# Performance work log

Hardware: AMD Instinct MI355X
Metric: run time of the kernel (lower is better)

Reference implementation:

```python
import jax, jax.numpy as jnp
import numpy as np

BLOCK = 128


def setup_inputs() -> dict:
    key = jax.random.key(0)
    k_x, k_w, k_s, k_b = jax.random.split(key, 4)
    B, S, IN, OUT = 2, 2048, 4096, 4096
    x = jax.random.normal(k_x, (B, S, IN), dtype=jnp.float32)
    # fp8-quantized weight values (simulate e4m3 rounding, keep fp32 storage)
    w = jax.random.normal(k_w, (OUT, IN), dtype=jnp.float32) * 0.02
    weight = w.astype(jnp.float8_e4m3fn).astype(jnp.float32)
    # per-128x128-block inverse scales
    weight_scale_inv = jax.random.uniform(
        k_s, (OUT // BLOCK, IN // BLOCK), dtype=jnp.float32, minval=0.5, maxval=1.5)
    bias = jax.random.normal(k_b, (OUT,), dtype=jnp.float32) * 0.01
    return {"x": x, "weight": weight, "weight_scale_inv": weight_scale_inv, "bias": bias}


def _dequant(weight, scale_inv):
    # weight: [O, I], scale_inv: [O/128, I/128] -> broadcast each scale over a 128x128 block
    O, I = weight.shape
    w = weight.reshape(O // BLOCK, BLOCK, I // BLOCK, BLOCK)
    w = w * scale_inv[:, None, :, None]
    return w.reshape(O, I)


def reference(x, weight, weight_scale_inv, bias):
    w_deq = _dequant(weight, weight_scale_inv)          # [O, I]
    out = jnp.einsum('bsi,oi->bso', x, w_deq)           # [B, S, O]
    return out + bias
```

## Files before the change

### kernel.cpp

```cpp
#include <hip/hip_runtime.h>
#include <hip/hip_bf16.h>
#include <stdint.h>

typedef __attribute__((ext_vector_type(4))) float f32x4;
typedef __attribute__((ext_vector_type(8))) short short8;

__device__ __forceinline__ ushort f2b(float f) {
    union { __hip_bfloat16 h; ushort u; } c;
    c.h = __float2bfloat16(f);
    return c.u;
}

__device__ __forceinline__ void gload_lds16(const void* g, void* lds) {
    __builtin_amdgcn_global_load_lds((const __attribute__((address_space(1))) void*)g,
                                     (__attribute__((address_space(3))) void*)lds,
                                     16, 0, 0);
}

#define BARRIER()  asm volatile("s_barrier" ::: "memory")
#define LGKM0()    asm volatile("s_waitcnt lgkmcnt(0)" ::: "memory")
#define VMCNT2()   asm volatile("s_waitcnt vmcnt(2)" ::: "memory")

__global__ void conv_x_kernel(const float* __restrict__ x, ushort* __restrict__ xb, long n8) {
    long i = (long)blockIdx.x * blockDim.x + threadIdx.x;
    if (i >= n8) return;
    const float4* xv = (const float4*)x;
    float4 v0 = xv[i * 2], v1 = xv[i * 2 + 1];
    short8 r;
    r[0] = (short)f2b(v0.x); r[1] = (short)f2b(v0.y); r[2] = (short)f2b(v0.z); r[3] = (short)f2b(v0.w);
    r[4] = (short)f2b(v1.x); r[5] = (short)f2b(v1.y); r[6] = (short)f2b(v1.z); r[7] = (short)f2b(v1.w);
    *(short8*)&xb[i * 8] = r;
}

__global__ void conv_w_kernel(const float* __restrict__ w, const float* __restrict__ sinv,
                              ushort* __restrict__ wb, int K, int nbk) {
    const int o = blockIdx.y;
    const int c = (blockIdx.x * blockDim.x + threadIdx.x) * 8;
    if (c >= K) return;
    const float s = sinv[(o >> 7) * nbk + (c >> 7)];
    const float4* wv = (const float4*)(w + (size_t)o * K + c);
    float4 v0 = wv[0], v1 = wv[1];
    short8 r;
    r[0] = (short)f2b(v0.x * s); r[1] = (short)f2b(v0.y * s); r[2] = (short)f2b(v0.z * s); r[3] = (short)f2b(v0.w * s);
    r[4] = (short)f2b(v1.x * s); r[5] = (short)f2b(v1.y * s); r[6] = (short)f2b(v1.z * s); r[7] = (short)f2b(v1.w * s);
    *(short8*)&wb[(size_t)o * K + c] = r;
}

__global__ __launch_bounds__(512, 2)
void gemm256_kernel(const ushort* __restrict__ A, const ushort* __restrict__ Bm,
                    const float* __restrict__ bias, float* __restrict__ C,
                    int M, int N, int K) {
    __shared__ alignas(16) short sm[2][32768];

    const int tid  = threadIdx.x;
    const int lane = tid & 63;
    const int wid  = tid >> 6;
    const int wr   = wid >> 2;
    const int wc   = wid & 3;
    const int nbn  = N >> 8;

    const int nwg = gridDim.x;
    const int swz = (blockIdx.x & 7) * (nwg >> 3) + (blockIdx.x >> 3);
    const int bm  = swz / nbn;
    const int bn  = swz % nbn;

    const short* gA = (const short*)A + (size_t)bm * 256 * K;
    const short* gB = (const short*)Bm + (size_t)bn * 256 * K;

    const int srow = wid * 8 + (lane >> 3);
    const int scol = ((lane & 7) ^ (lane >> 3)) << 3;

    auto STAGE_A = [&](int U, int kt, int buf) {
        const short* src = gA + (size_t)(U * 64 + srow) * K + kt * 64 + scol;
        gload_lds16(src, &sm[buf][U * 4096 + wid * 512]);
    };
    auto STAGE_B = [&](int U, int kt, int buf) {
        const short* src = gB + (size_t)(U * 64 + srow) * K + kt * 64 + scol;
        gload_lds16(src, &sm[buf][16384 + U * 4096 + wid * 512]);
    };

    auto LD_A = [&](const short* Ab, int mh, int kk, short8 (&a)[4]) {
#pragma unroll
        for (int m = 0; m < 4; ++m) {
            int row = wr * 128 + mh * 64 + m * 16 + (lane & 15);
            a[m] = *(const short8*)&Ab[row * 64 + ((kk * 32 + (lane >> 4) * 8) ^ ((lane & 7) << 3))];
        }
    };
    auto LD_B = [&](const short* Bb, int kk, short8 (&b)[4]) {
#pragma unroll
        for (int n = 0; n < 4; ++n) {
            int row = wc * 64 + n * 16 + (lane & 15);
            b[n] = *(const short8*)&Bb[row * 64 + ((kk * 32 + (lane >> 4) * 8) ^ ((lane & 7) << 3))];
        }
    };

    f32x4 acc[8][4] = {};

    const int nkt = K >> 6;

    {
#pragma unroll
        for (int U = 0; U < 4; ++U) STAGE_A(U, 0, 0);
#pragma unroll
        for (int U = 0; U < 4; ++U) STAGE_B(U, 0, 0);
        const int t1 = (nkt > 1) ? 1 : 0;
        STAGE_A(0, t1, 1);
        STAGE_A(2, t1, 1);
        VMCNT2();
        BARRIER();
    }

    for (int t = 0; t < nkt; ++t) {
        const int b  = t & 1;
        const short* Ab = &sm[b][0];
        const short* Bb = &sm[b][16384];
        const int tn  = (t + 1 < nkt) ? t + 1 : nkt - 1;
        const int tnn = (t + 2 < nkt) ? t + 2 : nkt - 1;

        short8 a0[4], a1[4], bf0[4], bf1[4];

        LD_A(Ab, 0, 0, a0);
        LD_B(Bb, 0, bf0);
        STAGE_B(0, tn, b ^ 1); STAGE_B(1, tn, b ^ 1); STAGE_B(2, tn, b ^ 1); STAGE_B(3, tn, b ^ 1);
        BARRIER();
        __builtin_amdgcn_s_setprio(1);
#pragma unroll
        for (int m = 0; m < 4; ++m)
#pragma unroll
            for (int n = 0; n < 4; ++n)
                acc[m][n] = __builtin_amdgcn_mfma_f32_16x16x32_bf16(a0[m], bf0[n], acc[m][n], 0, 0, 0);
        __builtin_amdgcn_s_setprio(0);
        LGKM0();
        BARRIER();

        LD_A(Ab, 1, 0, a1);
        STAGE_A(1, tn, b ^ 1); STAGE_A(3, tn, b ^ 1);
        BARRIER();
        __builtin_amdgcn_s_setprio(1);
#pragma unroll
        for (int m = 0; m < 4; ++m)
#pragma unroll
            for (int n = 0; n < 4; ++n)
                acc[4 + m][n] = __builtin_amdgcn_mfma_f32_16x16x32_bf16(a1[m], bf0[n], acc[4 + m][n], 0, 0, 0);
        __builtin_amdgcn_s_setprio(0);
        LGKM0();
        BARRIER();

        LD_A(Ab, 0, 1, a0);
        LD_B(Bb, 1, bf1);
        BARRIER();
        __builtin_amdgcn_s_setprio(1);
#pragma unroll
        for (int m = 0; m < 4; ++m)
#pragma unroll
            for (int n = 0; n < 4; ++n)
                acc[m][n] = __builtin_amdgcn_mfma_f32_16x16x32_bf16(a0[m], bf1[n], acc[m][n], 0, 0, 0);
        __builtin_amdgcn_s_setprio(0);
        LGKM0();
        BARRIER();

        LD_A(Ab, 1, 1, a1);
        STAGE_A(0, tnn, b); STAGE_A(2, tnn, b);
        BARRIER();
        __builtin_amdgcn_s_setprio(1);
#pragma unroll
        for (int m = 0; m < 4; ++m)
#pragma unroll
            for (int n = 0; n < 4; ++n)
                acc[4 + m][n] = __builtin_amdgcn_mfma_f32_16x16x32_bf16(a1[m], bf1[n], acc[4 + m][n], 0, 0, 0);
        __builtin_amdgcn_s_setprio(0);
        LGKM0();
        VMCNT2();
        BARRIER();
    }

    const int r0 = bm * 256 + wr * 128 + (lane >> 4) * 4;
    const int c0 = bn * 256 + wc * 64 + (lane & 15);
#pragma unroll
    for (int n = 0; n < 4; ++n) {
        float bv = bias[c0 + n * 16];
#pragma unroll
        for (int m = 0; m < 8; ++m) {
#pragma unroll
            for (int r = 0; r < 4; ++r) {
                C[(size_t)(r0 + m * 16 + r) * N + (c0 + n * 16)] = acc[m][n][r] + bv;
            }
        }
    }
}

__global__ void fallback_gemm(const float* __restrict__ x, const float* __restrict__ w,
                              const float* __restrict__ sinv, const float* __restrict__ bias,
                              float* __restrict__ out, int M, int N, int K) {
    int n = blockIdx.x * 64 + (threadIdx.x & 63);
    int m = blockIdx.y * 4 + (threadIdx.x >> 6);
    if (m >= M || n >= N) return;
    const int nbk = K >> 7;
    float acc = 0.f;
    for (int k = 0; k < K; ++k)
        acc += x[(size_t)m * K + k] * w[(size_t)n * K + k] * sinv[(n >> 7) * nbk + (k >> 7)];
    out[(size_t)m * N + n] = acc + bias[n];
}

extern "C" void kernel_launch(void* const* d_in, const int* in_sizes, int n_in,
                              void* d_out, int out_size, void* d_ws, size_t ws_size,
                              hipStream_t stream) {
    const float* x    = (const float*)d_in[0];
    const float* w    = (const float*)d_in[1];
    const float* sinv = (const float*)d_in[2];
    const float* bias = (const float*)d_in[3];
    float* out        = (float*)d_out;

    const int O = in_sizes[3];
    const int K = in_sizes[1] / O;
    const int M = (int)((long)in_sizes[0] / K);
    const int N = O;

    const size_t need = ((size_t)M * K + (size_t)N * K) * sizeof(ushort);
    const int nwg = (M / 256) * (N / 256);
    const bool ok = ws_size >= need && (M % 256 == 0) && (N % 256 == 0) &&
                    (K % 128 == 0) && (nwg % 8 == 0) && ((long)M * K % 2048 == 0) &&
                    (K % 2048 == 0);
    if (ok) {
        ushort* xb = (ushort*)d_ws;
        ushort* wb = xb + (size_t)M * K;
        long n8 = (long)M * K / 8;
        conv_x_kernel<<<dim3((unsigned)(n8 / 256)), 256, 0, stream>>>(x, xb, n8);
        conv_w_kernel<<<dim3(K / 2048, N), 256, 0, stream>>>(w, sinv, wb, K, K >> 7);
        gemm256_kernel<<<dim3(nwg), 512, 0, stream>>>(xb, wb, bias, out, M, N, K);
    } else {
        dim3 g(N / 64, (M + 3) / 4);
        fallback_gemm<<<g, 256, 0, stream>>>(x, w, sinv, bias, out, M, N, K);
    }
}
```

Baseline: 293.0 us.

## Fuse fp32-to-bf16 conversion and dequant scaling into GEMM tile loading

Removes the separate x and weight conversion kernels and the bf16 workspace. The GEMM now loads fp32 tiles through registers, applies the block scale, converts to bf16 and writes swizzled LDS, with loads software-pipelined across the four MFMA phases. This saves the extra kernel launches and the bf16 round trip through global memory. In exchange, each tile reads twice the global bytes, conversion runs inside the main loop, register pressure rises, and the direct global-to-LDS loads are lost.

```diff
diff --git a/kernel.cpp b/kernel.cpp
--- a/kernel.cpp
+++ b/kernel.cpp
@@ -11,45 +11,15 @@
     return c.u;
 }
 
-__device__ __forceinline__ void gload_lds16(const void* g, void* lds) {
-    __builtin_amdgcn_global_load_lds((const __attribute__((address_space(1))) void*)g,
-                                     (__attribute__((address_space(3))) void*)lds,
-                                     16, 0, 0);
-}
-
 #define BARRIER()  asm volatile("s_barrier" ::: "memory")
 #define LGKM0()    asm volatile("s_waitcnt lgkmcnt(0)" ::: "memory")
-#define VMCNT2()   asm volatile("s_waitcnt vmcnt(2)" ::: "memory")
-
-__global__ void conv_x_kernel(const float* __restrict__ x, ushort* __restrict__ xb, long n8) {
-    long i = (long)blockIdx.x * blockDim.x + threadIdx.x;
-    if (i >= n8) return;
-    const float4* xv = (const float4*)x;
-    float4 v0 = xv[i * 2], v1 = xv[i * 2 + 1];
-    short8 r;
-    r[0] = (short)f2b(v0.x); r[1] = (short)f2b(v0.y); r[2] = (short)f2b(v0.z); r[3] = (short)f2b(v0.w);
-    r[4] = (short)f2b(v1.x); r[5] = (short)f2b(v1.y); r[6] = (short)f2b(v1.z); r[7] = (short)f2b(v1.w);
-    *(short8*)&xb[i * 8] = r;
-}
-
-__global__ void conv_w_kernel(const float* __restrict__ w, const float* __restrict__ sinv,
-                              ushort* __restrict__ wb, int K, int nbk) {
-    const int o = blockIdx.y;
-    const int c = (blockIdx.x * blockDim.x + threadIdx.x) * 8;
-    if (c >= K) return;
-    const float s = sinv[(o >> 7) * nbk + (c >> 7)];
-    const float4* wv = (const float4*)(w + (size_t)o * K + c);
-    float4 v0 = wv[0], v1 = wv[1];
-    short8 r;
-    r[0] = (short)f2b(v0.x * s); r[1] = (short)f2b(v0.y * s); r[2] = (short)f2b(v0.z * s); r[3] = (short)f2b(v0.w * s);
-    r[4] = (short)f2b(v1.x * s); r[5] = (short)f2b(v1.y * s); r[6] = (short)f2b(v1.z * s); r[7] = (short)f2b(v1.w * s);
-    *(short8*)&wb[(size_t)o * K + c] = r;
-}
+
+struct U8 { float4 lo, hi; };
 
 __global__ __launch_bounds__(512, 2)
-void gemm256_kernel(const ushort* __restrict__ A, const ushort* __restrict__ Bm,
-                    const float* __restrict__ bias, float* __restrict__ C,
-                    int M, int N, int K) {
+void gemm256_fused_kernel(const float* __restrict__ X, const float* __restrict__ W,
+                          const float* __restrict__ sinv, const float* __restrict__ bias,
+                          float* __restrict__ C, int M, int N, int K, int nbk) {
     __shared__ alignas(16) short sm[2][32768];
 
     const int tid  = threadIdx.x;
@@ -63,20 +33,39 @@
     const int swz = (blockIdx.x & 7) * (nwg >> 3) + (blockIdx.x >> 3);
     const int bm  = swz / nbn;
     const int bn  = swz % nbn;
-
-    const short* gA = (const short*)A + (size_t)bm * 256 * K;
-    const short* gB = (const short*)Bm + (size_t)bn * 256 * K;
+    const int bn2 = bn * 2;
+
+    const float* gA = X + (size_t)bm * 256 * K;
+    const float* gB = W + (size_t)bn * 256 * K;
 
     const int srow = wid * 8 + (lane >> 3);
-    const int scol = ((lane & 7) ^ (lane >> 3)) << 3;
-
-    auto STAGE_A = [&](int U, int kt, int buf) {
-        const short* src = gA + (size_t)(U * 64 + srow) * K + kt * 64 + scol;
-        gload_lds16(src, &sm[buf][U * 4096 + wid * 512]);
-    };
-    auto STAGE_B = [&](int U, int kt, int buf) {
-        const short* src = gB + (size_t)(U * 64 + srow) * K + kt * 64 + scol;
-        gload_lds16(src, &sm[buf][16384 + U * 4096 + wid * 512]);
+    const int scl8 = (lane & 7) * 8;
+    const int wOff = (wid * 8 + (lane >> 3)) * 64 + ((((lane & 7) ^ (lane >> 3))) << 3);
+
+    auto LOAD_A = [&](int U, int kt) -> U8 {
+        const float* p = gA + (size_t)(U * 64 + srow) * K + kt * 64 + scl8;
+        U8 r; r.lo = *(const float4*)p; r.hi = *(const float4*)(p + 4); return r;
+    };
+    auto LOAD_B = [&](int U, int kt) -> U8 {
+        const float* p = gB + (size_t)(U * 64 + srow) * K + kt * 64 + scl8;
+        U8 r; r.lo = *(const float4*)p; r.hi = *(const float4*)(p + 4); return r;
+    };
+    auto WRITE_A = [&](int U, int buf, const U8& v) {
+        short8 r;
+        r[0] = (short)f2b(v.lo.x); r[1] = (short)f2b(v.lo.y);
+        r[2] = (short)f2b(v.lo.z); r[3] = (short)f2b(v.lo.w);
+        r[4] = (short)f2b(v.hi.x); r[5] = (short)f2b(v.hi.y);
+        r[6] = (short)f2b(v.hi.z); r[7] = (short)f2b(v.hi.w);
+        *(short8*)&sm[buf][U * 4096 + wOff] = r;
+    };
+    auto WRITE_B = [&](int U, int kt, int buf, const U8& v) {
+        const float s = sinv[(bn2 + (U >> 1)) * nbk + (kt >> 1)];
+        short8 r;
+        r[0] = (short)f2b(v.lo.x * s); r[1] = (short)f2b(v.lo.y * s);
+        r[2] = (short)f2b(v.lo.z * s); r[3] = (short)f2b(v.lo.w * s);
+        r[4] = (short)f2b(v.hi.x * s); r[5] = (short)f2b(v.hi.y * s);
+        r[6] = (short)f2b(v.hi.z * s); r[7] = (short)f2b(v.hi.w * s);
+        *(short8*)&sm[buf][16384 + U * 4096 + wOff] = r;
     };
 
     auto LD_A = [&](const short* Ab, int mh, int kk, short8 (&a)[4]) {
@@ -95,23 +84,22 @@
     };
 
     f32x4 acc[8][4] = {};
-
     const int nkt = K >> 6;
+    const int t1c = (nkt > 1) ? 1 : 0;
 
     {
-#pragma unroll
-        for (int U = 0; U < 4; ++U) STAGE_A(U, 0, 0);
-#pragma unroll
-        for (int U = 0; U < 4; ++U) STAGE_B(U, 0, 0);
-        const int t1 = (nkt > 1) ? 1 : 0;
-        STAGE_A(0, t1, 1);
-        STAGE_A(2, t1, 1);
-        VMCNT2();
-        BARRIER();
-    }
+        U8 u0 = LOAD_A(0, 0), u1 = LOAD_A(1, 0), u2 = LOAD_A(2, 0), u3 = LOAD_A(3, 0);
+        WRITE_A(0, 0, u0); WRITE_A(1, 0, u1); WRITE_A(2, 0, u2); WRITE_A(3, 0, u3);
+        u0 = LOAD_B(0, 0); u1 = LOAD_B(1, 0); u2 = LOAD_B(2, 0); u3 = LOAD_B(3, 0);
+        WRITE_B(0, 0, 0, u0); WRITE_B(1, 0, 0, u1); WRITE_B(2, 0, 0, u2); WRITE_B(3, 0, 0, u3);
+    }
+    U8 pB0 = LOAD_B(0, t1c), pB1 = LOAD_B(1, t1c);
+    LGKM0();
+    BARRIER();
 
     for (int t = 0; t < nkt; ++t) {
         const int b  = t & 1;
+        const int tb = b ^ 1;
         const short* Ab = &sm[b][0];
         const short* Bb = &sm[b][16384];
         const int tn  = (t + 1 < nkt) ? t + 1 : nkt - 1;
@@ -121,7 +109,8 @@
 
         LD_A(Ab, 0, 0, a0);
         LD_B(Bb, 0, bf0);
-        STAGE_B(0, tn, b ^ 1); STAGE_B(1, tn, b ^ 1); STAGE_B(2, tn, b ^ 1); STAGE_B(3, tn, b ^ 1);
+        U8 qB2 = LOAD_B(2, tn), qB3 = LOAD_B(3, tn);
+        WRITE_B(0, tn, tb, pB0); WRITE_B(1, tn, tb, pB1);
         BARRIER();
         __builtin_amdgcn_s_setprio(1);
 #pragma unroll
@@ -134,7 +123,8 @@
         BARRIER();
 
         LD_A(Ab, 1, 0, a1);
-        STAGE_A(1, tn, b ^ 1); STAGE_A(3, tn, b ^ 1);
+        U8 qA0 = LOAD_A(0, tn), qA1 = LOAD_A(1, tn);
+        WRITE_B(2, tn, tb, qB2); WRITE_B(3, tn, tb, qB3);
         BARRIER();
         __builtin_amdgcn_s_setprio(1);
 #pragma unroll
@@ -148,6 +138,8 @@
 
         LD_A(Ab, 0, 1, a0);
         LD_B(Bb, 1, bf1);
+        U8 qA2 = LOAD_A(2, tn), qA3 = LOAD_A(3, tn);
+        WRITE_A(0, tb, qA0); WRITE_A(1, tb, qA1);
         BARRIER();
         __builtin_amdgcn_s_setprio(1);
 #pragma unroll
@@ -160,7 +152,8 @@
         BARRIER();
 
         LD_A(Ab, 1, 1, a1);
-        STAGE_A(0, tnn, b); STAGE_A(2, tnn, b);
+        pB0 = LOAD_B(0, tnn); pB1 = LOAD_B(1, tnn);
+        WRITE_A(2, tb, qA2); WRITE_A(3, tb, qA3);
         BARRIER();
         __builtin_amdgcn_s_setprio(1);
 #pragma unroll
@@ -170,7 +163,6 @@
                 acc[4 + m][n] = __builtin_amdgcn_mfma_f32_16x16x32_bf16(a1[m], bf1[n], acc[4 + m][n], 0, 0, 0);
         __builtin_amdgcn_s_setprio(0);
         LGKM0();
-        VMCNT2();
         BARRIER();
     }
 
@@ -216,18 +208,11 @@
     const int M = (int)((long)in_sizes[0] / K);
     const int N = O;
 
-    const size_t need = ((size_t)M * K + (size_t)N * K) * sizeof(ushort);
     const int nwg = (M / 256) * (N / 256);
-    const bool ok = ws_size >= need && (M % 256 == 0) && (N % 256 == 0) &&
-                    (K % 128 == 0) && (nwg % 8 == 0) && ((long)M * K % 2048 == 0) &&
-                    (K % 2048 == 0);
+    const bool ok = (M % 256 == 0) && (N % 256 == 0) && (K % 128 == 0) && (nwg % 8 == 0);
     if (ok) {
-        ushort* xb = (ushort*)d_ws;
-        ushort* wb = xb + (size_t)M * K;
-        long n8 = (long)M * K / 8;
-        conv_x_kernel<<<dim3((unsigned)(n8 / 256)), 256, 0, stream>>>(x, xb, n8);
-        conv_w_kernel<<<dim3(K / 2048, N), 256, 0, stream>>>(w, sinv, wb, K, K >> 7);
-        gemm256_kernel<<<dim3(nwg), 512, 0, stream>>>(xb, wb, bias, out, M, N, K);
+        gemm256_fused_kernel<<<dim3(nwg), 512, 0, stream>>>(x, w, sinv, bias, out,
+                                                            M, N, K, K >> 7);
     } else {
         dim3 g(N / 64, (M + 3) / 4);
         fallback_gemm<<<g, 256, 0, stream>>>(x, w, sinv, bias, out, M, N, K);
```

Result: slower. 375.0 us (+28.0%).
